# Optimization experiments

Hardware: AMD Instinct MI355X
Metric: run time of the kernel (lower is better)

The kernel has to match this reference:

```python
import jax, jax.numpy as jnp
import numpy as np

N_NODES = 50000
N_EDGES = 800000
IN_DIM = 128
EDGE_DIM = 32
HID = 64


def _glorot(key, shape):
    fan_in, fan_out = shape[0], shape[1]
    lim = float(np.sqrt(6.0 / (fan_in + fan_out)))
    return jax.random.uniform(key, shape, jnp.float32, -lim, lim)


def setup_inputs() -> dict:
    key = jax.random.key(0)
    ks = jax.random.split(key, 16)
    x = jax.random.normal(ks[0], (N_NODES, IN_DIM), jnp.float32)
    edge_index = jax.random.randint(ks[1], (2, N_EDGES), 0, N_NODES, jnp.int64)
    edge_attr = jax.random.normal(ks[2], (N_EDGES, EDGE_DIM), jnp.float32)
    message = jax.random.normal(ks[3], (N_EDGES, HID), jnp.float32)
    return {
        "x": x,
        "edge_index": edge_index,
        "edge_attr": edge_attr,
        "message": message,
        "W_src": _glorot(ks[4], (IN_DIM, HID)),
        "W_dest": _glorot(ks[5], (IN_DIM, HID)),
        "W_edge": _glorot(ks[6], (EDGE_DIM, HID)),
        "attn_vec": _glorot(ks[7], (1, HID)),
        "mlp_w1": _glorot(ks[8], (2 * HID, HID)),
        "mlp_b1": jnp.zeros((HID,), jnp.float32),
        "bn1_g": jnp.ones((HID,), jnp.float32),
        "bn1_b": jnp.zeros((HID,), jnp.float32),
        "mlp_w2": _glorot(ks[9], (HID, HID)),
        "mlp_b2": jnp.zeros((HID,), jnp.float32),
        "bn2_g": jnp.ones((HID,), jnp.float32),
        "bn2_b": jnp.zeros((HID,), jnp.float32),
        "amlp_w": _glorot(ks[10], (HID, 1)),
        "amlp_b": jnp.zeros((1,), jnp.float32),
    }


def _batchnorm(h, g, b, eps=1e-5):
    mu = jnp.mean(h, axis=0)
    var = jnp.var(h, axis=0)  # biased, as torch BN training forward
    return (h - mu) * jax.lax.rsqrt(var + eps) * g + b


def _segment_softmax(scores, seg, num_segments):
    m = jax.ops.segment_max(scores, seg, num_segments=num_segments)
    m = jnp.where(jnp.isneginf(m), 0.0, m)
    e = jnp.exp(scores - m[seg])
    s = jax.ops.segment_sum(e, seg, num_segments=num_segments)
    return e / s[seg]


def _scatter_max0(vals, seg, num_segments):
    # torch_scatter reduce='max' fills empty segments with 0
    out = jax.ops.segment_max(vals, seg, num_segments=num_segments)
    return jnp.where(jnp.isneginf(out), 0.0, out)


def reference(x, edge_index, edge_attr, message, W_src, W_dest, W_edge, attn_vec,
              mlp_w1, mlp_b1, bn1_g, bn1_b, mlp_w2, mlp_b2, bn2_g, bn2_b,
              amlp_w, amlp_b):
    row, col = edge_index[0], edge_index[1]
    # attention scores per edge
    h = x[row] @ W_src + x[col] @ W_dest + edge_attr @ W_edge  # [E, H]
    scores = jax.nn.leaky_relu(h @ attn_vec[0], negative_slope=0.2)  # [E]
    attn = _segment_softmax(scores, col, N_NODES)  # [E]
    msg = message * attn[:, None]  # [E, H]
    fwd = _scatter_max0(msg, col, N_NODES)  # [N, H]
    bwd = _scatter_max0(msg, row, N_NODES)  # [N, H]
    out = jnp.concatenate([fwd, bwd], axis=1)  # [N, 2H]
    # node MLP (BatchNorm in training-stats mode, dropout disabled)
    h1 = jax.nn.relu(_batchnorm(out @ mlp_w1 + mlp_b1, bn1_g, bn1_b))
    h2 = jax.nn.relu(_batchnorm(h1 @ mlp_w2 + mlp_b2, bn2_g, bn2_b))
    gate = jax.nn.sigmoid(h2 @ amlp_w + amlp_b).reshape(-1)  # [N]
    return h2, gate
```

## Files before the change

kernel.cpp:

```cpp
#include <hip/hip_runtime.h>
#include <hip/hip_bf16.h>
#include <float.h>

#define IN_DIM 128
#define EDGE_DIM 32
#define HID 64
#define BKT_G 64
#define BCAP 3072
#define NBKT_MAX 784
#define CHUNK 4096

__global__ void k_uvw(const float* __restrict__ Wsrc, const float* __restrict__ Wdst,
                      const float* __restrict__ Wedge, const float* __restrict__ avec,
                      const int* __restrict__ ei32, int* sflag,
                      float* u, float* v, float* w,
                      int* gcur, float* stats, int nbkt) {
    int gt = blockIdx.x * blockDim.x + threadIdx.x;
    int gstride = gridDim.x * blockDim.x;
    for (int i = gt; i < 2 * nbkt; i += gstride) gcur[i] = 0;
    for (int i = gt; i < 512; i += gstride) stats[i] = 0.0f;
    if (gt == 0) {
        int odd_or = ei32[1] | ei32[3] | ei32[5] | ei32[7] | ei32[9] | ei32[11];
        sflag[0] = (odd_or == 0) ? 2 : 1;
    }
    int wave = gt >> 6;
    int lane = threadIdx.x & 63;
    const float* src; float* dst; int row;
    if (wave < 128)      { src = Wsrc;  dst = u; row = wave; }
    else if (wave < 256) { src = Wdst;  dst = v; row = wave - 128; }
    else if (wave < 288) { src = Wedge; dst = w; row = wave - 256; }
    else return;
    float acc = src[row * HID + lane] * avec[lane];
    for (int o = 32; o >= 1; o >>= 1) acc += __shfl_xor(acc, o);
    if (lane == 0) dst[row] = acc;
}

__global__ void k_pqdot(const float* __restrict__ x, const float* __restrict__ u,
                        const float* __restrict__ v,
                        const float* __restrict__ ea, const float* __restrict__ w,
                        float* p, float* q, float* rdot, int N, int E, int pqBlocks) {
    if ((int)blockIdx.x < pqBlocks) {
        int wave = (blockIdx.x * blockDim.x + threadIdx.x) >> 6;
        int lane = threadIdx.x & 63;
        if (wave >= N) return;
        const float* xr = x + (size_t)wave * IN_DIM;
        float a0 = xr[lane], a1 = xr[lane + 64];
        float pp = a0 * u[lane] + a1 * u[lane + 64];
        float qq = a0 * v[lane] + a1 * v[lane + 64];
        for (int m = 32; m >= 1; m >>= 1) { pp += __shfl_xor(pp, m); qq += __shfl_xor(qq, m); }
        if (lane == 0) { p[wave] = pp; q[wave] = qq; }
    } else {
        int gid = (blockIdx.x - pqBlocks) * blockDim.x + threadIdx.x;
        int e = gid >> 3;
        int j = gid & 7;
        if (e >= E) return;
        float4 av = ((const float4*)ea)[(size_t)e * 8 + j];
        float4 wv = ((const float4*)w)[j];
        float val = av.x * wv.x + av.y * wv.y + av.z * wv.z + av.w * wv.w;
        val += __shfl_xor(val, 4);
        val += __shfl_xor(val, 2);
        val += __shfl_xor(val, 1);
        if (j == 0) rdot[e] = val;
    }
}

__global__ __launch_bounds__(256) void k_binscore(const int* __restrict__ ei,
                                                  const int* __restrict__ sflag,
                                                  const float* __restrict__ rdot,
                                                  const float* __restrict__ p,
                                                  const float* __restrict__ q,
                                                  float* scores,
                                                  int* gcur_col, int* gcur_row,
                                                  unsigned* bbuf_col, unsigned* bbuf_row,
                                                  int E, int nbkt) {
    __shared__ int lc[NBKT_MAX], lrw[NBKT_MAX];
    __shared__ int gc[NBKT_MAX], grw[NBKT_MAX];
    int tid = threadIdx.x;
    int e0 = blockIdx.x * CHUNK;
    int e1 = e0 + CHUNK; if (e1 > E) e1 = E;
    for (int i = tid; i < nbkt; i += 256) { lc[i] = 0; lrw[i] = 0; }
    __syncthreads();
    int st = sflag[0];
    for (int e = e0 + tid; e < e1; e += 256) {
        int r = ei[(size_t)st * e];
        int c = ei[(size_t)st * (E + e)];
        float sc = rdot[e] + p[r] + q[c];
        scores[e] = (sc > 0.f) ? sc : 0.2f * sc;
        atomicAdd(&lc[c >> 6], 1);
        atomicAdd(&lrw[r >> 6], 1);
    }
    __syncthreads();
    for (int b = tid; b < nbkt; b += 256) {
        int n1 = lc[b];  if (n1) gc[b]  = atomicAdd(&gcur_col[b], n1);
        int n2 = lrw[b]; if (n2) grw[b] = atomicAdd(&gcur_row[b], n2);
        lc[b] = 0; lrw[b] = 0;
    }
    __syncthreads();
    for (int e = e0 + tid; e < e1; e += 256) {
        int r = ei[(size_t)st * e];
        int c = ei[(size_t)st * (E + e)];
        int pos = gc[c >> 6] + atomicAdd(&lc[c >> 6], 1);
        if (pos < BCAP) bbuf_col[(size_t)(c >> 6) * BCAP + pos] = (unsigned)((e << 6) | (c & 63));
        int pos2 = grw[r >> 6] + atomicAdd(&lrw[r >> 6], 1);
        if (pos2 < BCAP) bbuf_row[(size_t)(r >> 6) * BCAP + pos2] = (unsigned)((e << 6) | (r & 63));
    }
}

__global__ __launch_bounds__(512) void k_sortfwd(float* scores, const float* __restrict__ msg,
                                                 const int* __restrict__ bcur,
                                                 const unsigned* __restrict__ bbuf,
                                                 float* fwd, int N) {
    __shared__ unsigned raw[BCAP];
    __shared__ unsigned srt[BCAP];
    __shared__ float    ssc[BCAP];
    __shared__ int cnt[BKT_G], cur[BKT_G], sstart[BKT_G + 1];
    __shared__ int nodectr;
    int b = blockIdx.x, tid = threadIdx.x;
    int M = bcur[b]; if (M > BCAP) M = BCAP;
    if (tid < BKT_G) cnt[tid] = 0;
    if (tid == 0) nodectr = 0;
    __syncthreads();
    for (int i = tid; i < M; i += 512) {
        unsigned v = bbuf[(size_t)b * BCAP + i];
        raw[i] = v;
        atomicAdd(&cnt[v & 63], 1);
    }
    __syncthreads();
    if (tid < BKT_G) {
        int val = cnt[tid];
        int inc = val;
        for (int off = 1; off < BKT_G; off <<= 1) {
            int o = __shfl_up(inc, off);
            if (tid >= off) inc += o;
        }
        sstart[tid + 1] = inc;
        if (tid == 0) sstart[0] = 0;
        cur[tid] = inc - val;
    }
    __syncthreads();
    for (int j = tid; j < M; j += 512) {
        unsigned v = raw[j];
        int posn = atomicAdd(&cur[v & 63], 1);
        srt[posn] = v;
    }
    __syncthreads();
    for (int i = tid; i < M; i += 512) ssc[i] = scores[srt[i] >> 6];
    __syncthreads();
    int lane = tid & 63;
    while (true) {
        int n0;
        if (lane == 0) n0 = atomicAdd(&nodectr, 1);
        n0 = __shfl(n0, 0);
        if (n0 >= BKT_G) break;
        int node = b * BKT_G + n0;
        if (node >= N) continue;
        int a0 = sstart[n0], len = sstart[n0 + 1] - a0;
        if (len == 0) { fwd[(size_t)node * HID + lane] = 0.f; continue; }
        float m = -FLT_MAX;
        for (int k = lane; k < len; k += 64) m = fmaxf(m, ssc[a0 + k]);
        for (int o = 32; o >= 1; o >>= 1) m = fmaxf(m, __shfl_xor(m, o));
        float ssum = 0.f;
        for (int k = lane; k < len; k += 64) ssum += expf(ssc[a0 + k] - m);
        for (int o = 32; o >= 1; o >>= 1) ssum += __shfl_xor(ssum, o);
        float rcp = 1.f / ssum;
        for (int k = lane; k < len; k += 64) {
            int i = a0 + k;
            float at = expf(ssc[i] - m) * rcp;
            ssc[i] = at;
            scores[srt[i] >> 6] = at;
        }
        asm volatile("s_waitcnt lgkmcnt(0)" ::: "memory");
        float acc = -FLT_MAX;
        int k = 0;
        for (; k + 16 <= len; k += 16) {
            float vv[16];
#pragma unroll
            for (int u16 = 0; u16 < 16; u16++) {
                int i = a0 + k + u16;
                vv[u16] = msg[(size_t)(srt[i] >> 6) * HID + lane] * ssc[i];
            }
#pragma unroll
            for (int u16 = 0; u16 < 16; u16++) acc = fmaxf(acc, vv[u16]);
        }
        for (; k + 8 <= len; k += 8) {
            float vv[8];
#pragma unroll
            for (int u8 = 0; u8 < 8; u8++) {
                int i = a0 + k + u8;
                vv[u8] = msg[(size_t)(srt[i] >> 6) * HID + lane] * ssc[i];
            }
#pragma unroll
            for (int u8 = 0; u8 < 8; u8++) acc = fmaxf(acc, vv[u8]);
        }
        for (; k < len; k++) {
            int i = a0 + k;
            acc = fmaxf(acc, msg[(size_t)(srt[i] >> 6) * HID + lane] * ssc[i]);
        }
        fwd[(size_t)node * HID + lane] = acc;
    }
}

__global__ __launch_bounds__(512) void k_sortbwd(const float* __restrict__ scores,
                                                 const float* __restrict__ msg,
                                                 const int* __restrict__ bcur,
                                                 const unsigned* __restrict__ bbuf,
                                                 float* bwd, int N) {
    __shared__ unsigned raw[BCAP];
    __shared__ unsigned srt[BCAP];
    __shared__ float    ssc[BCAP];
    __shared__ int cnt[BKT_G], cur[BKT_G], sstart[BKT_G + 1];
    __shared__ int nodectr;
    int b = blockIdx.x, tid = threadIdx.x;
    int M = bcur[b]; if (M > BCAP) M = BCAP;
    if (tid < BKT_G) cnt[tid] = 0;
    if (tid == 0) nodectr = 0;
    __syncthreads();
    for (int i = tid; i < M; i += 512) {
        unsigned v = bbuf[(size_t)b * BCAP + i];
        raw[i] = v;
        atomicAdd(&cnt[v & 63], 1);
    }
    __syncthreads();
    if (tid < BKT_G) {
        int val = cnt[tid];
        int inc = val;
        for (int off = 1; off < BKT_G; off <<= 1) {
            int o = __shfl_up(inc, off);
            if (tid >= off) inc += o;
        }
        sstart[tid + 1] = inc;
        if (tid == 0) sstart[0] = 0;
        cur[tid] = inc - val;
    }
    __syncthreads();
    for (int j = tid; j < M; j += 512) {
        unsigned v = raw[j];
        int posn = atomicAdd(&cur[v & 63], 1);
        srt[posn] = v;
    }
    __syncthreads();
    for (int i = tid; i < M; i += 512) ssc[i] = scores[srt[i] >> 6];
    __syncthreads();
    int lane = tid & 63;
    while (true) {
        int n0;
        if (lane == 0) n0 = atomicAdd(&nodectr, 1);
        n0 = __shfl(n0, 0);
        if (n0 >= BKT_G) break;
        int node = b * BKT_G + n0;
        if (node >= N) continue;
        int a0 = sstart[n0], len = sstart[n0 + 1] - a0;
        if (len == 0) { bwd[(size_t)node * HID + lane] = 0.f; continue; }
        float acc = -FLT_MAX;
        int k = 0;
        for (; k + 16 <= len; k += 16) {
            float vv[16];
#pragma unroll
            for (int u16 = 0; u16 < 16; u16++) {
                int i = a0 + k + u16;
                vv[u16] = msg[(size_t)(srt[i] >> 6) * HID + lane] * ssc[i];
            }
#pragma unroll
            for (int u16 = 0; u16 < 16; u16++) acc = fmaxf(acc, vv[u16]);
        }
        for (; k + 8 <= len; k += 8) {
            float vv[8];
#pragma unroll
            for (int u8 = 0; u8 < 8; u8++) {
                int i = a0 + k + u8;
                vv[u8] = msg[(size_t)(srt[i] >> 6) * HID + lane] * ssc[i];
            }
#pragma unroll
            for (int u8 = 0; u8 < 8; u8++) acc = fmaxf(acc, vv[u8]);
        }
        for (; k < len; k++) {
            int i = a0 + k;
            acc = fmaxf(acc, msg[(size_t)(srt[i] >> 6) * HID + lane] * ssc[i]);
        }
        bwd[(size_t)node * HID + lane] = acc;
    }
}

__global__ __launch_bounds__(256) void k_mlp1(const float* __restrict__ fwd,
                                              const float* __restrict__ bwd,
                                              const float* __restrict__ W1,
                                              const float* __restrict__ b1,
                                              float* pre1, float* gsum, float* gss, int N) {
    __shared__ float lsum[HID], lss[HID];
    int t = threadIdx.x;
    if (t < HID) { lsum[t] = 0.f; lss[t] = 0.f; }
    __syncthreads();
    int h = t & 63, lr = t >> 6;
    float bh = b1[h];
    float s = 0.f, ssq = 0.f;
    for (int n = blockIdx.x * 4 + lr; n < N; n += gridDim.x * 4) {
        const float* fr = fwd + (size_t)n * HID;
        const float* br = bwd + (size_t)n * HID;
        float acc = bh;
        for (int k = 0; k < HID; k++) acc += fr[k] * W1[k * HID + h];
        for (int k = 0; k < HID; k++) acc += br[k] * W1[(HID + k) * HID + h];
        pre1[(size_t)n * HID + h] = acc;
        s += acc; ssq += acc * acc;
    }
    atomicAdd(&lsum[h], s);
    atomicAdd(&lss[h], ssq);
    __syncthreads();
    if (t < HID) { atomicAdd(&gsum[t], lsum[t]); atomicAdd(&gss[t], lss[t]); }
}

__global__ __launch_bounds__(256) void k_mlp2(const float* __restrict__ pre1,
                                              const float* __restrict__ gsum1,
                                              const float* __restrict__ gss1,
                                              const float* __restrict__ g1,
                                              const float* __restrict__ bb1,
                                              const float* __restrict__ W2,
                                              const float* __restrict__ b2v,
                                              float* pre2, float* gsum, float* gss, int N) {
    __shared__ float lsum[HID], lss[HID];
    __shared__ float sc1[HID], sh1[HID];
    int t = threadIdx.x;
    if (t < HID) {
        lsum[t] = 0.f; lss[t] = 0.f;
        float invN = 1.0f / (float)N;
        float mu = gsum1[t] * invN;
        float var = gss1[t] * invN - mu * mu;
        float rs = rsqrtf(var + 1e-5f);
        float s1 = rs * g1[t];
        sc1[t] = s1;
        sh1[t] = bb1[t] - mu * s1;
    }
    __syncthreads();
    int h = t & 63, lr = t >> 6;
    float bh = b2v[h];
    float s = 0.f, ssq = 0.f;
    for (int n = blockIdx.x * 4 + lr; n < N; n += gridDim.x * 4) {
        const float* pr = pre1 + (size_t)n * HID;
        float acc = bh;
        for (int k = 0; k < HID; k++) {
            float z = pr[k] * sc1[k] + sh1[k];
            z = (z > 0.f) ? z : 0.f;
            acc += z * W2[k * HID + h];
        }
        pre2[(size_t)n * HID + h] = acc;
        s += acc; ssq += acc * acc;
    }
    atomicAdd(&lsum[h], s);
    atomicAdd(&lss[h], ssq);
    __syncthreads();
    if (t < HID) { atomicAdd(&gsum[t], lsum[t]); atomicAdd(&gss[t], lss[t]); }
}

__global__ __launch_bounds__(256) void k_out(const float* __restrict__ pre2,
                                             const float* __restrict__ gsum2,
                                             const float* __restrict__ gss2,
                                             const float* __restrict__ g2,
                                             const float* __restrict__ bb2,
                                             const float* __restrict__ amw,
                                             const float* __restrict__ amb,
                                             float* out, int N) {
    __shared__ float sc2[HID], sh2[HID];
    int t = threadIdx.x;
    if (t < HID) {
        float invN = 1.0f / (float)N;
        float mu = gsum2[t] * invN;
        float var = gss2[t] * invN - mu * mu;
        float rs = rsqrtf(var + 1e-5f);
        float s2 = rs * g2[t];
        sc2[t] = s2;
        sh2[t] = bb2[t] - mu * s2;
    }
    __syncthreads();
    int gid = blockIdx.x * blockDim.x + t;
    int n = gid >> 6, h = gid & 63;
    if (n >= N) return;
    float z = pre2[(size_t)n * HID + h] * sc2[h] + sh2[h];
    float h2 = (z > 0.f) ? z : 0.f;
    out[(size_t)n * HID + h] = h2;
    float part = h2 * amw[h];
    for (int m = 32; m >= 1; m >>= 1) part += __shfl_xor(part, m);
    if (h == 0) {
        float gate = 1.0f / (1.0f + expf(-(part + amb[0])));
        out[(size_t)N * HID + n] = gate;
    }
}

extern "C" void kernel_launch(void* const* d_in, const int* in_sizes, int n_in,
                              void* d_out, int out_size, void* d_ws, size_t ws_size,
                              hipStream_t stream) {
    const float* x     = (const float*)d_in[0];
    const int*   ei    = (const int*)d_in[1];
    const float* ea    = (const float*)d_in[2];
    const float* msg   = (const float*)d_in[3];
    const float* Wsrc  = (const float*)d_in[4];
    const float* Wdst  = (const float*)d_in[5];
    const float* Wedge = (const float*)d_in[6];
    const float* avec  = (const float*)d_in[7];
    const float* W1    = (const float*)d_in[8];
    const float* b1    = (const float*)d_in[9];
    const float* g1    = (const float*)d_in[10];
    const float* bb1   = (const float*)d_in[11];
    const float* W2    = (const float*)d_in[12];
    const float* b2    = (const float*)d_in[13];
    const float* g2    = (const float*)d_in[14];
    const float* bb2   = (const float*)d_in[15];
    const float* amw   = (const float*)d_in[16];
    const float* amb   = (const float*)d_in[17];
    float* out = (float*)d_out;

    const int N = in_sizes[0] / IN_DIM;
    const int E = in_sizes[1] / 2;
    const int NH = N * HID;
    const int nbkt = (N + BKT_G - 1) / BKT_G;

    float* ws = (float*)d_ws;
    float* gsum1  = ws;
    float* gss1   = ws + 64;
    float* gsum2  = ws + 128;
    float* gss2   = ws + 192;
    int*   sflag  = (int*)(ws + 512);
    float* u      = ws + 576;
    float* v      = ws + 704;
    float* w      = ws + 832;
    float* T        = ws + 1024;
    float* p        = T;
    float* q        = p + N;
    float* scores   = q + N;
    float* rdot     = scores + E;
    int*   gcur_col = (int*)(rdot + E);
    int*   gcur_row = gcur_col + nbkt;
    unsigned* bbuf_col = (unsigned*)(gcur_row + nbkt);
    unsigned* bbuf_row = bbuf_col + (size_t)nbkt * BCAP;
    size_t T_words  = 2 * (size_t)N + 2 * (size_t)E + 2 * (size_t)nbkt
                    + 2 * (size_t)nbkt * BCAP;
    size_t T_sz     = (T_words < (size_t)NH) ? (size_t)NH : T_words;
    float* fwd  = ws + 1024 + T_sz;
    float* bwd  = fwd + (size_t)NH;
    float* pre1 = T;
    float* pre2 = fwd;

    const int pqBlocks   = (N * 64 + 255) / 256;
    const int edotBlocks = (E * 8 + 255) / 256;

    hipLaunchKernelGGL(k_uvw, dim3(72), dim3(256), 0, stream,
                       Wsrc, Wdst, Wedge, avec, ei, sflag, u, v, w,
                       gcur_col, ws, nbkt);
    hipLaunchKernelGGL(k_pqdot, dim3(pqBlocks + edotBlocks), dim3(256), 0, stream,
                       x, u, v, ea, w, p, q, rdot, N, E, pqBlocks);
    hipLaunchKernelGGL(k_binscore, dim3((E + CHUNK - 1) / CHUNK), dim3(256), 0, stream,
                       ei, sflag, rdot, p, q, scores,
                       gcur_col, gcur_row, bbuf_col, bbuf_row, E, nbkt);
    hipLaunchKernelGGL(k_sortfwd, dim3(nbkt), dim3(512), 0, stream,
                       scores, msg, gcur_col, bbuf_col, fwd, N);
    hipLaunchKernelGGL(k_sortbwd, dim3(nbkt), dim3(512), 0, stream,
                       scores, msg, gcur_row, bbuf_row, bwd, N);
    hipLaunchKernelGGL(k_mlp1, dim3(1024), dim3(256), 0, stream,
                       fwd, bwd, W1, b1, pre1, gsum1, gss1, N);
    hipLaunchKernelGGL(k_mlp2, dim3(1024), dim3(256), 0, stream,
                       pre1, gsum1, gss1, g1, bb1, W2, b2, pre2, gsum2, gss2, N);
    hipLaunchKernelGGL(k_out, dim3(pqBlocks), dim3(256), 0, stream,
                       pre2, gsum2, gss2, g2, bb2, amw, amb, out, N);
}
```

Measured before the change: 376.9 us.

## Use static node assignment in sort kernels and split MLP accumulators

The sort/scatter-max kernels drop the shared atomic work counter and instead give nodes to waves in a fixed stride of 8. They also remove the 16-wide unrolled gather loop, keeping only the 8-wide one, which lowers register pressure. The MLP kernels split each dot product across four independent accumulators with full unrolling, shortening the FMA dependency chain. Static assignment can unbalance work on skewed degree distributions, and the reordered summation changes floating-point rounding slightly.

```diff
diff --git a/kernel.cpp b/kernel.cpp
--- a/kernel.cpp
+++ b/kernel.cpp
@@ -114,11 +114,9 @@
     __shared__ unsigned srt[BCAP];
     __shared__ float    ssc[BCAP];
     __shared__ int cnt[BKT_G], cur[BKT_G], sstart[BKT_G + 1];
-    __shared__ int nodectr;
     int b = blockIdx.x, tid = threadIdx.x;
     int M = bcur[b]; if (M > BCAP) M = BCAP;
     if (tid < BKT_G) cnt[tid] = 0;
-    if (tid == 0) nodectr = 0;
     __syncthreads();
     for (int i = tid; i < M; i += 512) {
         unsigned v = bbuf[(size_t)b * BCAP + i];
@@ -146,15 +144,11 @@
     __syncthreads();
     for (int i = tid; i < M; i += 512) ssc[i] = scores[srt[i] >> 6];
     __syncthreads();
-    int lane = tid & 63;
-    while (true) {
-        int n0;
-        if (lane == 0) n0 = atomicAdd(&nodectr, 1);
-        n0 = __shfl(n0, 0);
-        if (n0 >= BKT_G) break;
-        int node = b * BKT_G + n0;
+    int wave = tid >> 6, lane = tid & 63;
+    for (int n = wave; n < BKT_G; n += 8) {
+        int node = b * BKT_G + n;
         if (node >= N) continue;
-        int a0 = sstart[n0], len = sstart[n0 + 1] - a0;
+        int a0 = sstart[n], len = sstart[n + 1] - a0;
         if (len == 0) { fwd[(size_t)node * HID + lane] = 0.f; continue; }
         float m = -FLT_MAX;
         for (int k = lane; k < len; k += 64) m = fmaxf(m, ssc[a0 + k]);
@@ -172,16 +166,6 @@
         asm volatile("s_waitcnt lgkmcnt(0)" ::: "memory");
         float acc = -FLT_MAX;
         int k = 0;
-        for (; k + 16 <= len; k += 16) {
-            float vv[16];
-#pragma unroll
-            for (int u16 = 0; u16 < 16; u16++) {
-                int i = a0 + k + u16;
-                vv[u16] = msg[(size_t)(srt[i] >> 6) * HID + lane] * ssc[i];
-            }
-#pragma unroll
-            for (int u16 = 0; u16 < 16; u16++) acc = fmaxf(acc, vv[u16]);
-        }
         for (; k + 8 <= len; k += 8) {
             float vv[8];
 #pragma unroll
@@ -209,11 +193,9 @@
     __shared__ unsigned srt[BCAP];
     __shared__ float    ssc[BCAP];
     __shared__ int cnt[BKT_G], cur[BKT_G], sstart[BKT_G + 1];
-    __shared__ int nodectr;
     int b = blockIdx.x, tid = threadIdx.x;
     int M = bcur[b]; if (M > BCAP) M = BCAP;
     if (tid < BKT_G) cnt[tid] = 0;
-    if (tid == 0) nodectr = 0;
     __syncthreads();
     for (int i = tid; i < M; i += 512) {
         unsigned v = bbuf[(size_t)b * BCAP + i];
@@ -241,28 +223,14 @@
     __syncthreads();
     for (int i = tid; i < M; i += 512) ssc[i] = scores[srt[i] >> 6];
     __syncthreads();
-    int lane = tid & 63;
-    while (true) {
-        int n0;
-        if (lane == 0) n0 = atomicAdd(&nodectr, 1);
-        n0 = __shfl(n0, 0);
-        if (n0 >= BKT_G) break;
-        int node = b * BKT_G + n0;
+    int wave = tid >> 6, lane = tid & 63;
+    for (int n = wave; n < BKT_G; n += 8) {
+        int node = b * BKT_G + n;
         if (node >= N) continue;
-        int a0 = sstart[n0], len = sstart[n0 + 1] - a0;
+        int a0 = sstart[n], len = sstart[n + 1] - a0;
         if (len == 0) { bwd[(size_t)node * HID + lane] = 0.f; continue; }
         float acc = -FLT_MAX;
         int k = 0;
-        for (; k + 16 <= len; k += 16) {
-            float vv[16];
-#pragma unroll
-            for (int u16 = 0; u16 < 16; u16++) {
-                int i = a0 + k + u16;
-                vv[u16] = msg[(size_t)(srt[i] >> 6) * HID + lane] * ssc[i];
-            }
-#pragma unroll
-            for (int u16 = 0; u16 < 16; u16++) acc = fmaxf(acc, vv[u16]);
-        }
         for (; k + 8 <= len; k += 8) {
             float vv[8];
 #pragma unroll
@@ -296,9 +264,22 @@
     for (int n = blockIdx.x * 4 + lr; n < N; n += gridDim.x * 4) {
         const float* fr = fwd + (size_t)n * HID;
         const float* br = bwd + (size_t)n * HID;
-        float acc = bh;
-        for (int k = 0; k < HID; k++) acc += fr[k] * W1[k * HID + h];
-        for (int k = 0; k < HID; k++) acc += br[k] * W1[(HID + k) * HID + h];
+        float a0 = bh, a1 = 0.f, a2 = 0.f, a3 = 0.f;
+#pragma unroll
+        for (int k = 0; k < HID; k += 4) {
+            a0 += fr[k]     * W1[k * HID + h];
+            a1 += fr[k + 1] * W1[(k + 1) * HID + h];
+            a2 += fr[k + 2] * W1[(k + 2) * HID + h];
+            a3 += fr[k + 3] * W1[(k + 3) * HID + h];
+        }
+#pragma unroll
+        for (int k = 0; k < HID; k += 4) {
+            a0 += br[k]     * W1[(HID + k) * HID + h];
+            a1 += br[k + 1] * W1[(HID + k + 1) * HID + h];
+            a2 += br[k + 2] * W1[(HID + k + 2) * HID + h];
+            a3 += br[k + 3] * W1[(HID + k + 3) * HID + h];
+        }
+        float acc = (a0 + a1) + (a2 + a3);
         pre1[(size_t)n * HID + h] = acc;
         s += acc; ssq += acc * acc;
     }
@@ -335,12 +316,19 @@
     float s = 0.f, ssq = 0.f;
     for (int n = blockIdx.x * 4 + lr; n < N; n += gridDim.x * 4) {
         const float* pr = pre1 + (size_t)n * HID;
-        float acc = bh;
-        for (int k = 0; k < HID; k++) {
-            float z = pr[k] * sc1[k] + sh1[k];
-            z = (z > 0.f) ? z : 0.f;
-            acc += z * W2[k * HID + h];
-        }
+        float a0 = bh, a1 = 0.f, a2 = 0.f, a3 = 0.f;
+#pragma unroll
+        for (int k = 0; k < HID; k += 4) {
+            float z0 = pr[k]     * sc1[k]     + sh1[k];     z0 = (z0 > 0.f) ? z0 : 0.f;
+            float z1 = pr[k + 1] * sc1[k + 1] + sh1[k + 1]; z1 = (z1 > 0.f) ? z1 : 0.f;
+            float z2 = pr[k + 2] * sc1[k + 2] + sh1[k + 2]; z2 = (z2 > 0.f) ? z2 : 0.f;
+            float z3 = pr[k + 3] * sc1[k + 3] + sh1[k + 3]; z3 = (z3 > 0.f) ? z3 : 0.f;
+            a0 += z0 * W2[k * HID + h];
+            a1 += z1 * W2[(k + 1) * HID + h];
+            a2 += z2 * W2[(k + 2) * HID + h];
+            a3 += z3 * W2[(k + 3) * HID + h];
+        }
+        float acc = (a0 + a1) + (a2 + a3);
         pre2[(size_t)n * HID + h] = acc;
         s += acc; ssq += acc * acc;
     }
```

Measured after the change: 307.8 us (median of 2 runs). 1.22x faster.
